# Optimization experiments

Hardware: AMD Instinct MI355X
Metric: run time of the kernel (lower is better)

Reference implementation:

```python
import jax, jax.numpy as jnp
import numpy as np
from jax import lax

H = 384
W = 384
N = H * W                 # flattened pixel count
N_LOC = N // 2            # unknown pixels with 3x3 matting-Laplacian stencils
KCM = 20                  # color-mixture KNN size
K_IU = 5                  # intra-unknown KNN size
NNZ_CM = N_LOC * KCM


def setup_inputs() -> dict:
    key = jax.random.key(0)
    ks = jax.random.split(key, 16)
    f32 = jnp.float32
    i32 = jnp.int32
    inp = {}
    inp["CM_weights"] = jax.random.uniform(ks[0], (N,), f32)
    inp["LOC_weights"] = jax.random.uniform(ks[1], (N,), f32)
    inp["IU_weights"] = jax.random.uniform(ks[2], (N,), f32)
    inp["KU_weights"] = jax.random.uniform(ks[3], (N,), f32)
    inp["lmbda"] = jnp.full((1,), 100.0, f32)
    inp["kToUconf"] = jax.random.uniform(ks[4], (N,), f32)
    inp["known"] = jax.random.uniform(ks[5], (N,), f32)
    inp["kToU"] = jax.random.uniform(ks[6], (N,), f32)
    inp["Wcm_data"] = jax.random.uniform(ks[7], (NNZ_CM,), f32)
    inp["LOC_flows"] = jax.random.uniform(ks[8], (9, 9, N_LOC), f32)
    inp["IU_flows"] = jax.random.uniform(ks[9], (N_LOC, K_IU), f32)
    inp["Wcm_row"] = jax.random.randint(ks[10], (NNZ_CM,), 0, N, dtype=i32)
    inp["Wcm_col"] = jax.random.randint(ks[11], (NNZ_CM,), 0, N, dtype=i32)
    # interior pixels so all 9 stencil neighbours are valid
    inp["LOC_inInd"] = jax.random.randint(ks[12], (N_LOC,), W + 1, N - W - 1, dtype=i32)
    inp["IU_inInd"] = jax.random.randint(ks[13], (N_LOC,), 0, N, dtype=i32)
    inp["IU_neighInd"] = jax.random.randint(ks[14], (N_LOC, K_IU), 0, N, dtype=i32)
    inp["width"] = W
    inp["cg_steps"] = 30
    return inp


def reference(CM_weights, LOC_weights, IU_weights, KU_weights, lmbda,
              kToUconf, known, kToU, Wcm_data, LOC_flows, IU_flows,
              Wcm_row, Wcm_col, LOC_inInd, IU_inInd, IU_neighInd,
              width, cg_steps):
    n = kToU.shape[0]
    seg = lambda v, i: jax.ops.segment_sum(v, i, num_segments=n)

    # --- color mixture: Wcm scaled by diag(CM_weights); L = diag(rowsum) - Wcm; Lcm = L^T L
    cm_vals = CM_weights[Wcm_row] * Wcm_data
    rs_cm = seg(cm_vals, Wcm_row)

    # --- matting Laplacian: 9x9 flows per unknown pixel over 3x3 stencil
    offs = jnp.array([-1 - width, -1, -1 + width, -width, 0, width,
                      1 - width, 1, 1 + width], dtype=LOC_inInd.dtype)
    neigh = LOC_inInd[:, None] + offs[None, :]                    # [n_loc, 9]
    fl = LOC_flows * LOC_weights[LOC_inInd][None, None, :]        # [9, 9, n_loc]
    nloc = neigh.shape[0]
    # entry (row=neigh[k,i], col=neigh[k,j]) has value fl[j, i, k]
    vals_m = jnp.transpose(fl, (2, 1, 0)).reshape(-1)
    rows_m = jnp.broadcast_to(neigh[:, :, None], (nloc, 9, 9)).reshape(-1)
    cols_m = jnp.broadcast_to(neigh[:, None, :], (nloc, 9, 9)).reshape(-1)
    rows_ms = jnp.concatenate([rows_m, cols_m])
    cols_ms = jnp.concatenate([cols_m, rows_m])
    vals_ms = 0.5 * jnp.concatenate([vals_m, vals_m])             # W = 0.5 (W + W^T)
    rs_m = seg(vals_ms, rows_ms)

    # --- intra-unknowns KNN affinities
    fiu = IU_flows * IU_weights[IU_inInd][:, None]                # [n_iu, K]
    rows_c0 = jnp.broadcast_to(IU_inInd[:, None], IU_neighInd.shape).reshape(-1)
    cols_c0 = IU_neighInd.reshape(-1)
    rows_cs = jnp.concatenate([rows_c0, cols_c0])
    cols_cs = jnp.concatenate([cols_c0, rows_c0])
    vals_cs = 0.5 * jnp.concatenate([fiu.reshape(-1), fiu.reshape(-1)])
    rs_c = seg(vals_cs, rows_cs)

    # --- diagonal data terms: KU + lmbda*known
    diag_ku = KU_weights * kToUconf + lmbda[0] * known
    b = diag_ku * kToU

    def matvec(v):
        # Lcm @ v = L^T (L v), keeping L in factored COO form
        Lv = rs_cm * v - seg(cm_vals * v[Wcm_col], Wcm_row)
        lcm = rs_cm * Lv - seg(cm_vals * Lv[Wcm_row], Wcm_col)
        lm = rs_m * v - seg(vals_ms * v[cols_ms], rows_ms)
        lc = rs_c * v - seg(vals_cs * v[cols_cs], rows_cs)
        return lcm + lm + lc + diag_ku * v

    def cg_step(carry, _):
        x, r, p, rs = carry
        Ap = matvec(p)
        alpha = rs / jnp.vdot(p, Ap)
        x = x + alpha * p
        r = r - alpha * Ap
        rs_new = jnp.vdot(r, r)
        p = r + (rs_new / rs) * p
        return (x, r, p, rs_new), None

    x0 = jnp.zeros_like(b)  # x0 = 0 as in MattingSolver
    (x, _, _, _), _ = lax.scan(cg_step, (x0, b, b, jnp.vdot(b, b)), None, length=cg_steps)
    return x
```

## Files before the change

### kernel.cpp

```cpp
#include <hip/hip_runtime.h>


#define TPB 256

__device__ __forceinline__ float blockReduce256(float v) {
  #pragma unroll
  for (int o = 32; o > 0; o >>= 1) v += __shfl_down(v, o, 64);
  __shared__ float s[4];
  int lane = threadIdx.x & 63, wv = threadIdx.x >> 6;
  if (lane == 0) s[wv] = v;
  __syncthreads();
  return (threadIdx.x == 0) ? (s[0] + s[1] + s[2] + s[3]) : 0.f;
}

__global__ void k_init0(const float* __restrict__ KUw, const float* __restrict__ kToUconf,
                        const float* __restrict__ lmbda, const float* __restrict__ known,
                        const float* __restrict__ kToU,
                        float* __restrict__ diag_ku, float2* __restrict__ PR,
                        float* __restrict__ x,
                        int* __restrict__ CNT, float* __restrict__ scal, int N)
{
  int i = blockIdx.x * TPB + threadIdx.x;
  if (i < 80) scal[i] = 0.f;
  if (i < 3 * N) CNT[i] = 0;
  float red = 0.f;
  if (i < N) {
    float dk = KUw[i] * kToUconf[i] + lmbda[0] * known[i];
    diag_ku[i] = dk;
    float b = dk * kToU[i];
    PR[i] = make_float2(b, b);
    x[i] = 0.f;
    red = b * b;
  }
  float v = blockReduce256(red);
  if (threadIdx.x == 0) atomicAdd(&scal[0], v);
}

__global__ void k_prep(float* __restrict__ LOC_flows, const int* __restrict__ LOC_inInd,
                       const float* __restrict__ LOCw, int NLOC)
{
  int k = blockIdx.x * TPB + threadIdx.x;
  float Fl[81];
  #pragma unroll
  for (int m = 0; m < 81; ++m) Fl[m] = LOC_flows[(size_t)m * NLOC + k];
  float hw = 0.5f * LOCw[LOC_inInd[k]];
  int idx = 0;
  #pragma unroll
  for (int a = 0; a < 9; ++a)
    #pragma unroll
    for (int b = a + 1; b < 9; ++b) {
      LOC_flows[(size_t)idx * NLOC + k] = hw * (Fl[a * 9 + b] + Fl[b * 9 + a]);
      ++idx;
    }
}

__global__ void k_hist(const int* __restrict__ Wrow, const int* __restrict__ Wcol,
                       const int* __restrict__ LOC_inInd, const int* __restrict__ width_p,
                       const int* __restrict__ IU_inInd, const int* __restrict__ IU_neighInd,
                       int* __restrict__ CNT,
                       unsigned short* __restrict__ tr, unsigned short* __restrict__ tc,
                       unsigned short* __restrict__ tU,
                       int NLOC, int N, int B0, int B1)
{
  int blk = blockIdx.x;
  if (blk < B0) {
    int e = blk * TPB + threadIdx.x;
    tr[e] = (unsigned short)atomicAdd(&CNT[Wrow[e]], 1);
    tc[e] = (unsigned short)atomicAdd(&CNT[N + Wcol[e]], 1);
  } else if (blk < B1) {
    int k = (blk - B0) * TPB + threadIdx.x;
    int wd = *width_p;
    int base = LOC_inInd[k];
    const int offs[9] = {-1 - wd, -1, -1 + wd, -wd, 0, wd, 1 - wd, 1, 1 + wd};
    #pragma unroll
    for (int a = 0; a < 9; ++a)
      tU[a * NLOC + k] = (unsigned short)atomicAdd(&CNT[2 * N + base + offs[a]], 1);
  } else {
    int k = (blk - B1) * TPB + threadIdx.x;
    tU[14 * NLOC + k] = (unsigned short)atomicAdd(&CNT[2 * N + IU_inInd[k]], 1);
    #pragma unroll
    for (int j = 0; j < 5; ++j)
      tU[(9 + j) * NLOC + k] =
          (unsigned short)atomicAdd(&CNT[2 * N + IU_neighInd[k * 5 + j]], 1);
  }
}

__global__ void k_scan1(int* __restrict__ OFF, int* __restrict__ bsum, int tot)
{
  __shared__ int s[TPB];
  int gid = blockIdx.x * TPB + threadIdx.x;
  int v = (gid < tot) ? OFF[gid] : 0;
  s[threadIdx.x] = v;
  __syncthreads();
  #pragma unroll
  for (int o = 1; o < TPB; o <<= 1) {
    int t = (threadIdx.x >= o) ? s[threadIdx.x - o] : 0;
    __syncthreads();
    s[threadIdx.x] += t;
    __syncthreads();
  }
  if (gid < tot) OFF[gid] = s[threadIdx.x] - v;
  if (threadIdx.x == TPB - 1) bsum[blockIdx.x] = s[threadIdx.x];
}

__global__ void k_scan2(int* __restrict__ bsum, int nPerArr)
{
  __shared__ int s[1024];
  int base = blockIdx.x * nPerArr;
  int v = (threadIdx.x < nPerArr) ? bsum[base + threadIdx.x] : 0;
  s[threadIdx.x] = v;
  __syncthreads();
  for (int o = 1; o < 1024; o <<= 1) {
    int t = (threadIdx.x >= o) ? s[threadIdx.x - o] : 0;
    __syncthreads();
    s[threadIdx.x] += t;
    __syncthreads();
  }
  if (threadIdx.x < nPerArr) bsum[base + threadIdx.x] = s[threadIdx.x] - v;
}

__global__ void k_scan3(int* __restrict__ OFF, const int* __restrict__ bsum, int tot)
{
  int gid = blockIdx.x * TPB + threadIdx.x;
  if (gid < tot) OFF[gid] += bsum[blockIdx.x];
}

__global__ void k_fill(const float* __restrict__ CMw, const float* __restrict__ Wcm_data,
                       const int* __restrict__ Wrow, const int* __restrict__ Wcol,
                       const int* __restrict__ LOC_inInd, const int* __restrict__ width_p,
                       const int* __restrict__ IU_inInd, const int* __restrict__ IU_neighInd,
                       const int* __restrict__ OFF,
                       const unsigned short* __restrict__ tr, const unsigned short* __restrict__ tc,
                       const unsigned short* __restrict__ tU,
                       int2* __restrict__ csrPk, int2* __restrict__ cscPk,
                       int* __restrict__ gU,
                       int NLOC, int N, int B0, int B1)
{
  int blk = blockIdx.x;
  if (blk < B0) {
    int e = blk * TPB + threadIdx.x;
    int row = Wrow[e], col = Wcol[e];
    int cv = __float_as_int(CMw[row] * Wcm_data[e]);
    csrPk[OFF[row] + tr[e]] = make_int2(col, cv);
    cscPk[OFF[N + col] + tc[e]] = make_int2(row, cv);
  } else if (blk < B1) {
    int k = (blk - B0) * TPB + threadIdx.x;
    int wd = *width_p;
    int base = LOC_inInd[k];
    const int offs[9] = {-1 - wd, -1, -1 + wd, -wd, 0, wd, 1 - wd, 1, 1 + wd};
    #pragma unroll
    for (int a = 0; a < 9; ++a)
      gU[OFF[2 * N + base + offs[a]] + tU[a * NLOC + k]] = a * NLOC + k;
  } else {
    int k = (blk - B1) * TPB + threadIdx.x;
    gU[OFF[2 * N + IU_inInd[k]] + tU[14 * NLOC + k]] = 14 * NLOC + k;
    #pragma unroll
    for (int j = 0; j < 5; ++j)
      gU[OFF[2 * N + IU_neighInd[k * 5 + j]] + tU[(9 + j) * NLOC + k]] =
          (9 + j) * NLOC + k;
  }
}

__global__ void k_it1(const float2* __restrict__ PR,
                      const float* __restrict__ S2, const int* __restrict__ LOC_inInd,
                      const int* __restrict__ width_p,
                      const float* __restrict__ IU_flows, const int* __restrict__ IU_inInd,
                      const int* __restrict__ IU_neighInd, const float* __restrict__ IUw,
                      const float* __restrict__ diag_ku,
                      const int* __restrict__ OFF, const int2* __restrict__ csrPk,
                      float* __restrict__ u_all,
                      float* __restrict__ Lv, float* __restrict__ rs_cm,
                      const float* __restrict__ rsN, const float* __restrict__ rsO, int first,
                      float* __restrict__ pAp_t,
                      int NNZ, int NLOC, int N, int B0, int B1)
{
  int blk = blockIdx.x;
  float beta = first ? 0.f : rsN[0] / rsO[0];
  float red = 0.f;
  if (blk < B0) {
    int k = blk * TPB + threadIdx.x;
    int wd = *width_p;
    int base = LOC_inInd[k];
    const int offs[9] = {-1 - wd, -1, -1 + wd, -wd, 0, wd, 1 - wd, 1, 1 + wd};
    float pv[9];
    #pragma unroll
    for (int a = 0; a < 9; ++a) {
      float2 pr = PR[base + offs[a]];
      pv[a] = __builtin_fmaf(beta, pr.x, pr.y);
    }
    float u[9] = {0.f, 0.f, 0.f, 0.f, 0.f, 0.f, 0.f, 0.f, 0.f};
    float qf = 0.f;
    int idx = 0;
    #pragma unroll
    for (int a = 0; a < 9; ++a)
      #pragma unroll
      for (int b = a + 1; b < 9; ++b) {
        float sv = S2[(size_t)idx * NLOC + k];
        ++idx;
        float d = pv[a] - pv[b];
        float t = sv * d;
        u[a] += t; u[b] -= t;
        qf += t * d;
      }
    #pragma unroll
    for (int a = 0; a < 9; ++a) u_all[a * NLOC + k] = u[a];
    red = qf;
  } else if (blk < B1) {
    int k = (blk - B0) * TPB + threadIdx.x;
    int r0 = IU_inInd[k];
    float hw = 0.5f * IUw[r0];
    float2 prr = PR[r0];
    float pr = __builtin_fmaf(beta, prr.x, prr.y);
    int c[5]; float w[5];
    #pragma unroll
    for (int j = 0; j < 5; ++j) {
      c[j] = IU_neighInd[k * 5 + j];
      w[j] = hw * IU_flows[k * 5 + j];
    }
    float pc[5];
    #pragma unroll
    for (int j = 0; j < 5; ++j) {
      float2 pp = PR[c[j]];
      pc[j] = __builtin_fmaf(beta, pp.x, pp.y);
    }
    float qf = 0.f, asum = 0.f;
    #pragma unroll
    for (int j = 0; j < 5; ++j) {
      float d = pr - pc[j];
      float uA = w[j] * d;
      u_all[(9 + j) * NLOC + k] = -uA;
      asum += uA;
      qf += uA * d;
    }
    u_all[14 * NLOC + k] = asum;
    red = qf;
  } else {
    int i = (blk - B1) * TPB + threadIdx.x;
    float2 pri = PR[i];
    float pi = __builtin_fmaf(beta, pri.x, pri.y);
    int s = OFF[i];
    int e = (i == N - 1) ? NNZ : OFF[i + 1];
    float acc = 0.f, rs = 0.f;
    int q = s;
    for (; q + 8 <= e; q += 8) {
      int2 ed[8];
      #pragma unroll
      for (int m = 0; m < 8; ++m) ed[m] = csrPk[q + m];
      float g[8];
      #pragma unroll
      for (int m = 0; m < 8; ++m) {
        float2 pp = PR[ed[m].x];
        g[m] = __builtin_fmaf(beta, pp.x, pp.y);
      }
      #pragma unroll
      for (int m = 0; m < 8; ++m) {
        float cv = __int_as_float(ed[m].y);
        rs += cv;
        acc += cv * (pi - g[m]);
      }
    }
    for (; q + 4 <= e; q += 4) {
      int2 ed[4];
      #pragma unroll
      for (int m = 0; m < 4; ++m) ed[m] = csrPk[q + m];
      float g[4];
      #pragma unroll
      for (int m = 0; m < 4; ++m) {
        float2 pp = PR[ed[m].x];
        g[m] = __builtin_fmaf(beta, pp.x, pp.y);
      }
      #pragma unroll
      for (int m = 0; m < 4; ++m) {
        float cv = __int_as_float(ed[m].y);
        rs += cv;
        acc += cv * (pi - g[m]);
      }
    }
    for (; q < e; ++q) {
      int2 ed = csrPk[q];
      float cv = __int_as_float(ed.y);
      float2 pp = PR[ed.x];
      rs += cv;
      acc += cv * (pi - __builtin_fmaf(beta, pp.x, pp.y));
    }
    Lv[i] = acc;
    rs_cm[i] = rs;
    red = diag_ku[i] * pi * pi + acc * acc;
  }
  float v = blockReduce256(red);
  if (threadIdx.x == 0) atomicAdd(pAp_t, v);
}

__global__ void k_it2(float* __restrict__ x, float2* __restrict__ PR,
                      const float* __restrict__ Lv,
                      const float* __restrict__ rs_cm, const float* __restrict__ diag_ku,
                      const int* __restrict__ OFF,
                      const int2* __restrict__ cscPk,
                      const int* __restrict__ gU, const float* __restrict__ u_all,
                      const float* __restrict__ rs_t, const float* __restrict__ pAp_t,
                      const float* __restrict__ rsO, int first,
                      float* __restrict__ rs_t1,
                      int NNZ, int NLOC, int N)
{
  int i = blockIdx.x * TPB + threadIdx.x;
  float alpha = rs_t[0] / pAp_t[0];
  float beta = first ? 0.f : rs_t[0] / rsO[0];
  float tg = 0.f;
  {
    int s0 = OFF[2 * N + i];
    int e0 = (i == N - 1) ? 15 * NLOC : OFF[2 * N + i + 1];
    int q = s0;
    for (; q + 8 <= e0; q += 8) {
      int g[8];
      #pragma unroll
      for (int m = 0; m < 8; ++m) g[m] = gU[q + m];
      float u[8];
      #pragma unroll
      for (int m = 0; m < 8; ++m) u[m] = u_all[g[m]];
      #pragma unroll
      for (int m = 0; m < 8; ++m) tg += u[m];
    }
    for (; q + 4 <= e0; q += 4) {
      int g[4];
      #pragma unroll
      for (int m = 0; m < 4; ++m) g[m] = gU[q + m];
      float u[4];
      #pragma unroll
      for (int m = 0; m < 4; ++m) u[m] = u_all[g[m]];
      #pragma unroll
      for (int m = 0; m < 4; ++m) tg += u[m];
    }
    for (; q < e0; ++q) tg += u_all[gU[q]];
  }
  float sc = 0.f;
  {
    int s0 = OFF[N + i];
    int e0 = (i == N - 1) ? NNZ : OFF[N + i + 1];
    int q = s0;
    for (; q + 8 <= e0; q += 8) {
      int2 ed[8];
      #pragma unroll
      for (int m = 0; m < 8; ++m) ed[m] = cscPk[q + m];
      float l[8];
      #pragma unroll
      for (int m = 0; m < 8; ++m) l[m] = Lv[ed[m].x];
      #pragma unroll
      for (int m = 0; m < 8; ++m) sc += __int_as_float(ed[m].y) * l[m];
    }
    for (; q + 4 <= e0; q += 4) {
      int2 ed[4];
      #pragma unroll
      for (int m = 0; m < 4; ++m) ed[m] = cscPk[q + m];
      float l[4];
      #pragma unroll
      for (int m = 0; m < 4; ++m) l[m] = Lv[ed[m].x];
      #pragma unroll
      for (int m = 0; m < 4; ++m) sc += __int_as_float(ed[m].y) * l[m];
    }
    for (; q < e0; ++q) {
      int2 ed = cscPk[q];
      sc += __int_as_float(ed.y) * Lv[ed.x];
    }
  }
  float2 pri = PR[i];
  float pi = __builtin_fmaf(beta, pri.x, pri.y);
  float Ap = diag_ku[i] * pi + rs_cm[i] * Lv[i] - sc + tg;
  x[i] += alpha * pi;
  float rn = pri.y - alpha * Ap;
  PR[i] = make_float2(pi, rn);
  float v = blockReduce256(rn * rn);
  if (threadIdx.x == 0) atomicAdd(rs_t1, v);
}

extern "C" void kernel_launch(void* const* d_in, const int* in_sizes, int n_in,
                              void* d_out, int out_size, void* d_ws, size_t ws_size,
                              hipStream_t stream)
{
  const float* CMw       = (const float*)d_in[0];
  const float* LOCw      = (const float*)d_in[1];
  const float* IUw       = (const float*)d_in[2];
  const float* KUw       = (const float*)d_in[3];
  const float* lmbda     = (const float*)d_in[4];
  const float* kToUconf  = (const float*)d_in[5];
  const float* known     = (const float*)d_in[6];
  const float* kToU      = (const float*)d_in[7];
  const float* Wcm_data  = (const float*)d_in[8];
  float*       LOC_flows = (float*)d_in[9];
  const float* IU_flows  = (const float*)d_in[10];
  const int*   Wrow      = (const int*)d_in[11];
  const int*   Wcol      = (const int*)d_in[12];
  const int*   LOC_inInd = (const int*)d_in[13];
  const int*   IU_inInd  = (const int*)d_in[14];
  const int*   IU_neighInd = (const int*)d_in[15];
  const int*   width_p   = (const int*)d_in[16];
  const int CG_STEPS = 30;

  const int N    = in_sizes[0];
  const int NNZ  = in_sizes[8];
  const int NLOC = in_sizes[13];

  float* x       = (float*)d_out;
  float2* PR     = (float2*)d_ws;
  float* Lv      = (float*)(PR + (size_t)N);
  float* rs_cm   = Lv + N;
  float* diag_ku = rs_cm + N;
  int2*  csrPk   = (int2*)(diag_ku + N);
  int2*  cscPk   = csrPk + (size_t)NNZ;
  int*   gU      = (int*)(cscPk + (size_t)NNZ);
  int*   OFF     = gU + (size_t)15 * NLOC;
  unsigned short* tr = (unsigned short*)(OFF + (size_t)3 * N);
  unsigned short* tc = tr + (size_t)NNZ;
  unsigned short* tU = tc + (size_t)NNZ;
  float* u_all   = (float*)tr;
  int*   bsum    = (int*)(tU + (size_t)15 * NLOC);
  float* scal    = (float*)(bsum + 3 * (N / TPB));

  const int Bn = N / TPB;
  const int Bz = NNZ / TPB;
  const int Bl = NLOC / TPB;
  const int Z3 = 3 * Bn;

  k_init0<<<Z3, TPB, 0, stream>>>(KUw, kToUconf, lmbda, known, kToU,
                                  diag_ku, PR, x, OFF, scal, N);
  k_prep<<<Bl, TPB, 0, stream>>>(LOC_flows, LOC_inInd, LOCw, NLOC);
  k_hist<<<Bz + 2 * Bl, TPB, 0, stream>>>(Wrow, Wcol, LOC_inInd, width_p,
                                          IU_inInd, IU_neighInd, OFF,
                                          tr, tc, tU, NLOC, N, Bz, Bz + Bl);
  k_scan1<<<Z3, TPB, 0, stream>>>(OFF, bsum, 3 * N);
  k_scan2<<<3, 1024, 0, stream>>>(bsum, Bn);
  k_scan3<<<Z3, TPB, 0, stream>>>(OFF, bsum, 3 * N);
  k_fill<<<Bz + 2 * Bl, TPB, 0, stream>>>(CMw, Wcm_data, Wrow, Wcol,
                                          LOC_inInd, width_p, IU_inInd, IU_neighInd,
                                          OFF, tr, tc, tU,
                                          csrPk, cscPk, gU,
                                          NLOC, N, Bz, Bz + Bl);

  for (int t = 0; t < CG_STEPS; ++t) {
    const float* rsN = scal + t;
    const float* rsO = scal + (t == 0 ? 0 : t - 1);
    k_it1<<<2 * Bl + Bn, TPB, 0, stream>>>(
        PR, LOC_flows, LOC_inInd, width_p,
        IU_flows, IU_inInd, IU_neighInd, IUw,
        diag_ku, OFF, csrPk, u_all, Lv, rs_cm,
        rsN, rsO, (t == 0) ? 1 : 0, scal + 40 + t,
        NNZ, NLOC, N, Bl, 2 * Bl);
    k_it2<<<Bn, TPB, 0, stream>>>(
        x, PR, Lv, rs_cm, diag_ku, OFF, cscPk, gU, u_all,
        rsN, scal + 40 + t, rsO, (t == 0) ? 1 : 0, scal + t + 1,
        NNZ, NLOC, N);
  }
}
```

Baseline: 1.812 ms.

## Sort matting-Laplacian stencil entries by pixel bucket for gather locality

Adds a counting sort of the unknown-pixel stencil centres into 256-pixel buckets. It builds a permutation, permutes the packed pairwise flow coefficients into a spare region of LOC_flows, and renumbers the stencil entries in the histogram, fill and CG kernels. Neighbouring threads then gather nearby PR entries and scatter to nearby gU slots, which should improve cache locality in the 30 CG iterations. In exchange it adds four setup kernels and a one-time copy of 36 coefficient planes.

```diff
diff --git a/kernel.cpp b/kernel.cpp
--- a/kernel.cpp
+++ b/kernel.cpp
@@ -18,10 +18,12 @@
                         const float* __restrict__ kToU,
                         float* __restrict__ diag_ku, float2* __restrict__ PR,
                         float* __restrict__ x,
-                        int* __restrict__ CNT, float* __restrict__ scal, int N)
+                        int* __restrict__ CNT, int* __restrict__ sCNT,
+                        float* __restrict__ scal, int N)
 {
   int i = blockIdx.x * TPB + threadIdx.x;
   if (i < 80) scal[i] = 0.f;
+  if (i < 576) sCNT[i] = 0;
   if (i < 3 * N) CNT[i] = 0;
   float red = 0.f;
   if (i < N) {
@@ -54,8 +56,51 @@
     }
 }
 
+__global__ void k_sh(const int* __restrict__ LOC_inInd, int* __restrict__ sCNT,
+                     unsigned short* __restrict__ sTick, int NLOC)
+{
+  int k = blockIdx.x * TPB + threadIdx.x;
+  sTick[k] = (unsigned short)atomicAdd(&sCNT[LOC_inInd[k] >> 8], 1);
+}
+
+__global__ void k_ss(int* __restrict__ sCNT)
+{
+  __shared__ int s[576];
+  int v = sCNT[threadIdx.x];
+  s[threadIdx.x] = v;
+  __syncthreads();
+  for (int o = 1; o < 576; o <<= 1) {
+    int t = (threadIdx.x >= o) ? s[threadIdx.x - o] : 0;
+    __syncthreads();
+    s[threadIdx.x] += t;
+    __syncthreads();
+  }
+  sCNT[threadIdx.x] = s[threadIdx.x] - v;
+}
+
+__global__ void k_sc(const int* __restrict__ LOC_inInd, const int* __restrict__ sCNT,
+                     const unsigned short* __restrict__ sTick,
+                     int* __restrict__ perm, int* __restrict__ LOC_inIndP, int NLOC)
+{
+  int k = blockIdx.x * TPB + threadIdx.x;
+  int v = LOC_inInd[k];
+  int pos = sCNT[v >> 8] + sTick[k];
+  perm[pos] = k;
+  LOC_inIndP[pos] = v;
+}
+
+__global__ void k_permS2(float* __restrict__ LOC_flows, const int* __restrict__ perm,
+                         int NLOC)
+{
+  int kp = blockIdx.x * TPB + threadIdx.x;
+  int k = perm[kp];
+  #pragma unroll
+  for (int m = 0; m < 36; ++m)
+    LOC_flows[(size_t)(36 + m) * NLOC + kp] = LOC_flows[(size_t)m * NLOC + k];
+}
+
 __global__ void k_hist(const int* __restrict__ Wrow, const int* __restrict__ Wcol,
-                       const int* __restrict__ LOC_inInd, const int* __restrict__ width_p,
+                       const int* __restrict__ LOC_inIndP, const int* __restrict__ width_p,
                        const int* __restrict__ IU_inInd, const int* __restrict__ IU_neighInd,
                        int* __restrict__ CNT,
                        unsigned short* __restrict__ tr, unsigned short* __restrict__ tc,
@@ -68,13 +113,13 @@
     tr[e] = (unsigned short)atomicAdd(&CNT[Wrow[e]], 1);
     tc[e] = (unsigned short)atomicAdd(&CNT[N + Wcol[e]], 1);
   } else if (blk < B1) {
-    int k = (blk - B0) * TPB + threadIdx.x;
+    int kp = (blk - B0) * TPB + threadIdx.x;
     int wd = *width_p;
-    int base = LOC_inInd[k];
+    int base = LOC_inIndP[kp];
     const int offs[9] = {-1 - wd, -1, -1 + wd, -wd, 0, wd, 1 - wd, 1, 1 + wd};
     #pragma unroll
     for (int a = 0; a < 9; ++a)
-      tU[a * NLOC + k] = (unsigned short)atomicAdd(&CNT[2 * N + base + offs[a]], 1);
+      tU[a * NLOC + kp] = (unsigned short)atomicAdd(&CNT[2 * N + base + offs[a]], 1);
   } else {
     int k = (blk - B1) * TPB + threadIdx.x;
     tU[14 * NLOC + k] = (unsigned short)atomicAdd(&CNT[2 * N + IU_inInd[k]], 1);
@@ -127,7 +172,7 @@
 
 __global__ void k_fill(const float* __restrict__ CMw, const float* __restrict__ Wcm_data,
                        const int* __restrict__ Wrow, const int* __restrict__ Wcol,
-                       const int* __restrict__ LOC_inInd, const int* __restrict__ width_p,
+                       const int* __restrict__ LOC_inIndP, const int* __restrict__ width_p,
                        const int* __restrict__ IU_inInd, const int* __restrict__ IU_neighInd,
                        const int* __restrict__ OFF,
                        const unsigned short* __restrict__ tr, const unsigned short* __restrict__ tc,
@@ -144,13 +189,13 @@
     csrPk[OFF[row] + tr[e]] = make_int2(col, cv);
     cscPk[OFF[N + col] + tc[e]] = make_int2(row, cv);
   } else if (blk < B1) {
-    int k = (blk - B0) * TPB + threadIdx.x;
+    int kp = (blk - B0) * TPB + threadIdx.x;
     int wd = *width_p;
-    int base = LOC_inInd[k];
+    int base = LOC_inIndP[kp];
     const int offs[9] = {-1 - wd, -1, -1 + wd, -wd, 0, wd, 1 - wd, 1, 1 + wd};
     #pragma unroll
     for (int a = 0; a < 9; ++a)
-      gU[OFF[2 * N + base + offs[a]] + tU[a * NLOC + k]] = a * NLOC + k;
+      gU[OFF[2 * N + base + offs[a]] + tU[a * NLOC + kp]] = a * NLOC + kp;
   } else {
     int k = (blk - B1) * TPB + threadIdx.x;
     gU[OFF[2 * N + IU_inInd[k]] + tU[14 * NLOC + k]] = 14 * NLOC + k;
@@ -162,7 +207,7 @@
 }
 
 __global__ void k_it1(const float2* __restrict__ PR,
-                      const float* __restrict__ S2, const int* __restrict__ LOC_inInd,
+                      const float* __restrict__ S2p, const int* __restrict__ LOC_inIndP,
                       const int* __restrict__ width_p,
                       const float* __restrict__ IU_flows, const int* __restrict__ IU_inInd,
                       const int* __restrict__ IU_neighInd, const float* __restrict__ IUw,
@@ -178,9 +223,9 @@
   float beta = first ? 0.f : rsN[0] / rsO[0];
   float red = 0.f;
   if (blk < B0) {
-    int k = blk * TPB + threadIdx.x;
+    int kp = blk * TPB + threadIdx.x;
     int wd = *width_p;
-    int base = LOC_inInd[k];
+    int base = LOC_inIndP[kp];
     const int offs[9] = {-1 - wd, -1, -1 + wd, -wd, 0, wd, 1 - wd, 1, 1 + wd};
     float pv[9];
     #pragma unroll
@@ -195,7 +240,7 @@
     for (int a = 0; a < 9; ++a)
       #pragma unroll
       for (int b = a + 1; b < 9; ++b) {
-        float sv = S2[(size_t)idx * NLOC + k];
+        float sv = S2p[(size_t)idx * NLOC + kp];
         ++idx;
         float d = pv[a] - pv[b];
         float t = sv * d;
@@ -203,7 +248,7 @@
         qf += t * d;
       }
     #pragma unroll
-    for (int a = 0; a < 9; ++a) u_all[a * NLOC + k] = u[a];
+    for (int a = 0; a < 9; ++a) u_all[a * NLOC + kp] = u[a];
     red = qf;
   } else if (blk < B1) {
     int k = (blk - B0) * TPB + threadIdx.x;
@@ -414,6 +459,10 @@
   float* u_all   = (float*)tr;
   int*   bsum    = (int*)(tU + (size_t)15 * NLOC);
   float* scal    = (float*)(bsum + 3 * (N / TPB));
+  int*   perm    = (int*)(scal + 80);
+  int*   LOC_inIndP = perm + NLOC;
+  int*   sCNT    = LOC_inIndP + NLOC;
+  unsigned short* sTick = (unsigned short*)(sCNT + 576);
 
   const int Bn = N / TPB;
   const int Bz = NNZ / TPB;
@@ -421,25 +470,30 @@
   const int Z3 = 3 * Bn;
 
   k_init0<<<Z3, TPB, 0, stream>>>(KUw, kToUconf, lmbda, known, kToU,
-                                  diag_ku, PR, x, OFF, scal, N);
+                                  diag_ku, PR, x, OFF, sCNT, scal, N);
   k_prep<<<Bl, TPB, 0, stream>>>(LOC_flows, LOC_inInd, LOCw, NLOC);
-  k_hist<<<Bz + 2 * Bl, TPB, 0, stream>>>(Wrow, Wcol, LOC_inInd, width_p,
+  k_sh<<<Bl, TPB, 0, stream>>>(LOC_inInd, sCNT, sTick, NLOC);
+  k_ss<<<1, 576, 0, stream>>>(sCNT);
+  k_sc<<<Bl, TPB, 0, stream>>>(LOC_inInd, sCNT, sTick, perm, LOC_inIndP, NLOC);
+  k_permS2<<<Bl, TPB, 0, stream>>>(LOC_flows, perm, NLOC);
+  k_hist<<<Bz + 2 * Bl, TPB, 0, stream>>>(Wrow, Wcol, LOC_inIndP, width_p,
                                           IU_inInd, IU_neighInd, OFF,
                                           tr, tc, tU, NLOC, N, Bz, Bz + Bl);
   k_scan1<<<Z3, TPB, 0, stream>>>(OFF, bsum, 3 * N);
   k_scan2<<<3, 1024, 0, stream>>>(bsum, Bn);
   k_scan3<<<Z3, TPB, 0, stream>>>(OFF, bsum, 3 * N);
   k_fill<<<Bz + 2 * Bl, TPB, 0, stream>>>(CMw, Wcm_data, Wrow, Wcol,
-                                          LOC_inInd, width_p, IU_inInd, IU_neighInd,
+                                          LOC_inIndP, width_p, IU_inInd, IU_neighInd,
                                           OFF, tr, tc, tU,
                                           csrPk, cscPk, gU,
                                           NLOC, N, Bz, Bz + Bl);
 
+  const float* S2p = LOC_flows + (size_t)36 * NLOC;
   for (int t = 0; t < CG_STEPS; ++t) {
     const float* rsN = scal + t;
     const float* rsO = scal + (t == 0 ? 0 : t - 1);
     k_it1<<<2 * Bl + Bn, TPB, 0, stream>>>(
-        PR, LOC_flows, LOC_inInd, width_p,
+        PR, S2p, LOC_inIndP, width_p,
         IU_flows, IU_inInd, IU_neighInd, IUw,
         diag_ku, OFF, csrPk, u_all, Lv, rs_cm,
         rsN, rsO, (t == 0) ? 1 : 0, scal + 40 + t,
```

New measurement: 1.781 ms. Within noise of the previous version (-1.7%).
